# Optimization experiments

Hardware: AMD Instinct MI355X
Metric: run time of the kernel (lower is better)

## Reference

```python
import jax, jax.numpy as jnp
import numpy as np
from jax import lax

C, K, G = 256, 3, 8
CG = C // G          # group channels
P = K * K            # sampling points per group
STRIDE, PAD, DIL = 1, 1, 1
OFFSET_SCALE = 1.0
EPS = 1e-5


def setup_inputs() -> dict:
    key = jax.random.key(0)
    ks = jax.random.split(key, 8)
    N, H, W = 4, 64, 64
    return {
        "x": jax.random.normal(ks[0], (N, C, H, W), jnp.float32),
        "dw_w": jax.random.normal(ks[1], (C, 1, K, K), jnp.float32) * 0.1,
        "dw_b": jax.random.normal(ks[2], (C,), jnp.float32) * 0.01,
        "gn_g": jnp.ones((C,), jnp.float32),
        "gn_b": jnp.zeros((C,), jnp.float32),
        "off_w": jax.random.normal(ks[3], (C, G * P * 2), jnp.float32) * 0.01,
        "off_b": jax.random.normal(ks[4], (G * P * 2,), jnp.float32) * 0.1,
        "mask_w": jax.random.normal(ks[5], (C, G * P), jnp.float32) * 0.02,
        "mask_b": jax.random.normal(ks[6], (G * P,), jnp.float32) * 0.02,
    }


def _dcnv3_core(x_nhwc, offset, mask):
    # x_nhwc (N,H,W,C); offset (N,Ho,Wo,G*P*2); mask (N,Ho,Wo,G*P) already softmaxed
    inp = jnp.pad(x_nhwc, ((0, 0), (PAD, PAD), (PAD, PAD), (0, 0)))
    N, Hp, Wp, _ = inp.shape
    Ho = (Hp - (DIL * (K - 1) + 1)) // STRIDE + 1
    Wo = (Wp - (DIL * (K - 1) + 1)) // STRIDE + 1
    base = (DIL * (K - 1)) // 2 + 0.5
    ref_y = (base + jnp.arange(Ho, dtype=jnp.float32) * STRIDE) / Hp  # (Ho,)
    ref_x = (base + jnp.arange(Wo, dtype=jnp.float32) * STRIDE) / Wp  # (Wo,)
    # dilation grid; flatten order p = iw*K + ih (matches torch meshgrid(x,y) ij)
    kvals = jnp.arange(K, dtype=jnp.float32) * DIL - (DIL * (K - 1)) // 2
    gx = jnp.repeat(kvals, K) / Wp  # (P,)
    gy = jnp.tile(kvals, K) / Hp    # (P,)
    off = offset.reshape(N, Ho, Wo, G, P, 2)
    # normalized sampling locations in [0,1] (then grid_sample convention 2*loc-1)
    loc_x = ref_x[None, None, :, None, None] + gx * OFFSET_SCALE + off[..., 0] * OFFSET_SCALE / Wp
    loc_y = ref_y[None, :, None, None, None] + gy * OFFSET_SCALE + off[..., 1] * OFFSET_SCALE / Hp
    # pixel coords, align_corners=False: px = loc*size - 0.5
    px = loc_x * Wp - 0.5
    py = loc_y * Hp - 0.5
    x0 = jnp.floor(px)
    y0 = jnp.floor(py)
    wx = px - x0
    wy = py - y0
    x0i = x0.astype(jnp.int32)
    y0i = y0.astype(jnp.int32)

    inp_flat = inp.reshape(N, Hp * Wp, G, CG)
    n_idx = jnp.arange(N)[:, None, None, None, None]
    g_idx = jnp.arange(G)[None, None, None, :, None]

    def gather(yi, xi):
        # zeros padding: clamp index, zero out-of-bounds corners
        valid = (yi >= 0) & (yi < Hp) & (xi >= 0) & (xi < Wp)
        idx = jnp.clip(yi, 0, Hp - 1) * Wp + jnp.clip(xi, 0, Wp - 1)
        v = inp_flat[n_idx, idx, g_idx]  # (N,Ho,Wo,G,P,CG)
        return v * valid[..., None]

    m = mask.reshape(N, Ho, Wo, G, P)
    out = jnp.zeros((N, Ho, Wo, G, CG), jnp.float32)
    for dy, dx, w in ((0, 0, (1 - wy) * (1 - wx)), (0, 1, (1 - wy) * wx),
                      (1, 0, wy * (1 - wx)), (1, 1, wy * wx)):
        v = gather(y0i + dy, x0i + dx)
        out = out + jnp.einsum('nhwgp,nhwgpc->nhwgc', m * w, v)
    return out.reshape(N, Ho, Wo, G * CG)


def reference(x, dw_w, dw_b, gn_g, gn_b, off_w, off_b, mask_w, mask_b):
    N, _, H, W = x.shape
    # depthwise 3x3 conv (groups=channels)
    x1 = lax.conv_general_dilated(
        x, dw_w, (1, 1), [((K - 1) // 2, (K - 1) // 2)] * 2,
        dimension_numbers=('NCHW', 'OIHW', 'NCHW'), feature_group_count=C)
    x1 = x1 + dw_b[None, :, None, None]
    # GroupNorm with num_groups=1: normalize over (C,H,W) per sample
    mu = jnp.mean(x1, axis=(1, 2, 3), keepdims=True)
    var = jnp.mean((x1 - mu) ** 2, axis=(1, 2, 3), keepdims=True)
    x1 = (x1 - mu) * lax.rsqrt(var + EPS)
    x1 = x1 * gn_g[None, :, None, None] + gn_b[None, :, None, None]
    x1 = jax.nn.gelu(x1, approximate=False)
    x1 = jnp.transpose(x1, (0, 2, 3, 1))  # NHWC
    offset = x1 @ off_w + off_b                                  # (N,H,W,G*P*2)
    mask = jax.nn.softmax((x1 @ mask_w + mask_b).reshape(N, H, W, G, P), axis=-1)
    mask = mask.reshape(N, H, W, G * P)
    out = _dcnv3_core(jnp.transpose(x, (0, 2, 3, 1)), offset, mask)
    return jnp.transpose(out, (0, 3, 1, 2))  # back to NCHW
```

## Files before the change

kernel.cpp:

```cpp
#include <hip/hip_runtime.h>
#include <math.h>

#define NB   4
#define CH   256
#define HW   4096
#define NCOL 216
#define MTOT 16384
#define CHW  1048576
#define EPSV 1e-5f

#define OFF_NHWC 0
#define NHWCSZ   (NB*HW*CH/2)
#define OFF_OM   (OFF_NHWC + NHWCSZ)
#define OMSZ     (MTOT*NCOL/2)
#define OFF_AB   (OFF_OM + OMSZ)
#define ABSZ     (MTOT*CH/2)
#define OFF_WB   (OFF_AB + ABSZ)
#define WBSZ     (CH*CH/2)
#define OFF_BI   (OFF_WB + WBSZ)
#define OFF_PT   (OFF_BI + 256)

typedef short bf16x8 __attribute__((ext_vector_type(8)));
typedef float f32x4  __attribute__((ext_vector_type(4)));

__device__ __forceinline__ unsigned short f2bf(float f) {
    unsigned int u = __builtin_bit_cast(unsigned int, f);
    u += 0x7fffu + ((u >> 16) & 1u);
    return (unsigned short)(u >> 16);
}

__device__ __forceinline__ float bf2f(unsigned short s) {
    return __builtin_bit_cast(float, (unsigned int)s << 16);
}

__global__ __launch_bounds__(256) void conv_prep_kernel(
    const float* __restrict__ x, const float* __restrict__ dw_w,
    const float* __restrict__ dw_b,
    const float* __restrict__ off_w, const float* __restrict__ off_b,
    const float* __restrict__ mask_w, const float* __restrict__ mask_b,
    unsigned short* __restrict__ A, unsigned short* __restrict__ inp_nhwc,
    unsigned short* __restrict__ Wc_bt, float* __restrict__ bias,
    float* __restrict__ partials) {
    __shared__ float xs[32 * 108];
    __shared__ unsigned short tb[32 * 36];
    __shared__ float rs1[256], rs2[256];
    int b = blockIdx.x;
    int tid = threadIdx.x;
    if (b < 256) {
        int k = b, n = tid;
        float v = 0.f;
        if (n < 144)      v = off_w[k * 144 + n];
        else if (n < 216) v = mask_w[k * 72 + (n - 144)];
        Wc_bt[(size_t)n * 256 + k] = f2bf(v);
        if (b == 0) {
            float bb = 0.f;
            if (n < 144)      bb = off_b[n];
            else if (n < 216) bb = mask_b[n - 144];
            bias[n] = bb;
        }
    }
    int ct  = b & 7;
    int hwt = (b >> 3) & 127;
    int n   = b >> 10;
    int c0 = ct * 32;
    int hw0 = hwt * 32;
    int h  = hw0 >> 6;
    int w0 = hw0 & 63;
    const float* xb = x + ((size_t)n * CH + c0) * HW;
    for (int it = 0; it < 13; ++it) {
        int q = it * 256 + tid;
        if (q < 3264) {
            int cl = q / 102;
            int rr = q - cl * 102;
            int r  = rr / 34;
            int i  = rr - r * 34;
            int gh = h - 1 + r;
            int gw = w0 - 1 + i;
            float v = 0.f;
            if (gh >= 0 && gh < 64 && gw >= 0 && gw < 64)
                v = xb[(size_t)cl * HW + gh * 64 + gw];
            xs[cl * 108 + r * 36 + i] = v;
        }
    }
    __syncthreads();
    int wl = tid & 31;
    int cbase = (tid >> 5) * 4;
    float s1 = 0.f, s2 = 0.f;
    ushort4 o;
    unsigned short ov[4];
#pragma unroll
    for (int j = 0; j < 4; ++j) {
        int c = c0 + cbase + j;
        float acc = dw_b[c];
        const float* wk = dw_w + c * 9;
#pragma unroll
        for (int r = 0; r < 3; ++r)
#pragma unroll
            for (int kx = 0; kx < 3; ++kx)
                acc = fmaf(xs[(cbase + j) * 108 + r * 36 + wl + kx], wk[r * 3 + kx], acc);
        s1 += acc; s2 += acc * acc;
        ov[j] = f2bf(acc);
    }
    o.x = ov[0]; o.y = ov[1]; o.z = ov[2]; o.w = ov[3];
    *(ushort4*)&tb[wl * 36 + cbase] = o;
    rs1[tid] = s1; rs2[tid] = s2;
    {
        int r2 = tid >> 3, cg = tid & 7;
        ushort4 rv;
        rv.x = f2bf(xs[(cg * 4 + 0) * 108 + 36 + r2 + 1]);
        rv.y = f2bf(xs[(cg * 4 + 1) * 108 + 36 + r2 + 1]);
        rv.z = f2bf(xs[(cg * 4 + 2) * 108 + 36 + r2 + 1]);
        rv.w = f2bf(xs[(cg * 4 + 3) * 108 + 36 + r2 + 1]);
        *(ushort4*)&inp_nhwc[((size_t)(n * HW + hw0 + r2)) * 256 + c0 + cg * 4] = rv;
    }
    __syncthreads();
    for (int s = 128; s > 0; s >>= 1) {
        if (tid < s) { rs1[tid] += rs1[tid + s]; rs2[tid] += rs2[tid + s]; }
        __syncthreads();
    }
    if (tid == 0) {
        partials[2 * b]     = rs1[0];
        partials[2 * b + 1] = rs2[0];
    }
    int r2 = tid >> 3, cg = tid & 7;
    ushort4 w4 = *(const ushort4*)&tb[r2 * 36 + cg * 4];
    *(ushort4*)&A[((size_t)(n * HW + hw0 + r2)) * 256 + c0 + cg * 4] = w4;
}

#define LDK 72
__global__ __launch_bounds__(256) void gemm_fused_kernel(
    const unsigned short* __restrict__ A, const unsigned short* __restrict__ Bt,
    const float* __restrict__ bias, const float* __restrict__ partials,
    const float* __restrict__ gn_g, const float* __restrict__ gn_b,
    unsigned short* __restrict__ offmask) {
    __shared__ unsigned short As[32 * LDK];
    __shared__ unsigned short Bs[256 * LDK];
    __shared__ float red1[256], red2[256];
    int m0 = blockIdx.x * 32;
    int n = m0 >> 12;
    int tid = threadIdx.x, lane = tid & 63, wid = tid >> 6;
    float s1 = 0.f, s2 = 0.f;
    for (int i = tid; i < 1024; i += 256) {
        s1 += partials[2 * (n * 1024 + i)];
        s2 += partials[2 * (n * 1024 + i) + 1];
    }
    red1[tid] = s1; red2[tid] = s2;
    __syncthreads();
    for (int st = 128; st > 0; st >>= 1) {
        if (tid < st) { red1[tid] += red1[tid + st]; red2[tid] += red2[tid + st]; }
        __syncthreads();
    }
    float mean = red1[0] * (1.f / (float)CHW);
    float var  = red2[0] * (1.f / (float)CHW) - mean * mean;
    float rsig = rsqrtf(var + EPSV);
    f32x4 acc[2][4] = {};
    for (int k0 = 0; k0 < 256; k0 += 64) {
        {
            int row = tid >> 3, kk0 = (tid & 7) * 8;
            union { uint4 u; unsigned short s[8]; } in, ou;
            in.u = *(const uint4*)&A[((size_t)(m0 + row)) * 256 + k0 + kk0];
#pragma unroll
            for (int j = 0; j < 8; ++j) {
                int ch = k0 + kk0 + j;
                float v = bf2f(in.s[j]);
                v = (v - mean) * rsig * gn_g[ch] + gn_b[ch];
                v = 0.5f * v * (1.0f + erff(v * 0.70710678118654752f));
                ou.s[j] = f2bf(v);
            }
            *(uint4*)&As[row * LDK + kk0] = ou.u;
        }
#pragma unroll
        for (int i = 0; i < 8; ++i) {
            int q = i * 256 + tid;
            int mm = q >> 3, kk = (q & 7) * 8;
            *(uint4*)&Bs[mm * LDK + kk] = *(const uint4*)&Bt[(size_t)mm * 256 + k0 + kk];
        }
        __syncthreads();
#pragma unroll
        for (int kh = 0; kh < 2; ++kh) {
            bf16x8 af[2], bfr[4];
#pragma unroll
            for (int mi = 0; mi < 2; ++mi)
                af[mi] = *(const bf16x8*)&As[(mi * 16 + (lane & 15)) * LDK + kh * 32 + (lane >> 4) * 8];
#pragma unroll
            for (int nj = 0; nj < 4; ++nj)
                bfr[nj] = *(const bf16x8*)&Bs[(wid * 64 + nj * 16 + (lane & 15)) * LDK + kh * 32 + (lane >> 4) * 8];
#pragma unroll
            for (int mi = 0; mi < 2; ++mi)
#pragma unroll
                for (int nj = 0; nj < 4; ++nj)
                    acc[mi][nj] = __builtin_amdgcn_mfma_f32_16x16x32_bf16(
                        af[mi], bfr[nj], acc[mi][nj], 0, 0, 0);
        }
        __syncthreads();
    }
#pragma unroll
    for (int nj = 0; nj < 4; ++nj) {
        int col = wid * 64 + nj * 16 + (lane & 15);
        if (col < NCOL) {
            float bcol = bias[col];
#pragma unroll
            for (int mi = 0; mi < 2; ++mi)
#pragma unroll
                for (int r = 0; r < 4; ++r) {
                    int row = m0 + mi * 16 + (lane >> 4) * 4 + r;
                    offmask[(size_t)row * NCOL + col] = f2bf(acc[mi][nj][r] + bcol);
                }
        }
    }
}

__global__ __launch_bounds__(256) void dcn_out_kernel(
    const unsigned short* __restrict__ inp_nhwc, const unsigned short* __restrict__ offmask,
    float* __restrict__ out) {
    __shared__ float lom[16 * 216];
    __shared__ float ot[16 * 260];
    int tid = threadIdx.x, lane = tid & 63, wid = tid >> 6;
    int pix0 = blockIdx.x * 16;
    int n = pix0 >> 12;
    int hwb = pix0 & 4095;
    {
        const unsigned int* om2 = (const unsigned int*)(offmask + (size_t)pix0 * NCOL);
        for (int i = tid; i < 16 * NCOL / 2; i += 256) {
            unsigned int v = om2[i];
            lom[2 * i]     = bf2f((unsigned short)(v & 0xffffu));
            lom[2 * i + 1] = bf2f((unsigned short)(v >> 16));
        }
    }
    __syncthreads();
    int ph = lane >> 5;
    int l  = lane & 31;
    int g  = l >> 2;
    int ch0 = l * 8;
    const unsigned short* base = inp_nhwc + (size_t)n * HW * 256;
#pragma unroll
    for (int it = 0; it < 2; ++it) {
        int pixloc = it * 8 + wid * 2 + ph;
        int hw = hwb + pixloc;
        int h = hw >> 6, w = hw & 63;
        const float* lm = &lom[pixloc * NCOL];
        float lg[9];
        float mx = -1e30f;
#pragma unroll
        for (int p = 0; p < 9; ++p) { lg[p] = lm[144 + g * 9 + p]; mx = fmaxf(mx, lg[p]); }
        float sum = 0.f;
#pragma unroll
        for (int p = 0; p < 9; ++p) { lg[p] = __expf(lg[p] - mx); sum += lg[p]; }
        float rs = 1.0f / sum;
        float acc[8] = {};
#pragma unroll
        for (int p = 0; p < 9; ++p) {
            float ox = lm[g * 18 + p * 2];
            float oy = lm[g * 18 + p * 2 + 1];
            float px = (float)(w + (p / 3)) + ox;
            float py = (float)(h + (p % 3)) + oy;
            float xf = floorf(px), yf = floorf(py);
            float wx = px - xf, wy = py - yf;
            int x0 = (int)xf, y0 = (int)yf;
            float m = lg[p] * rs;
            float w00 = m * (1.f - wy) * (1.f - wx);
            float w01 = m * (1.f - wy) * wx;
            float w10 = m * wy * (1.f - wx);
            float w11 = m * wy * wx;
#pragma unroll
            for (int corner = 0; corner < 4; ++corner) {
                int yi = y0 + (corner >> 1);
                int xi = x0 + (corner & 1);
                float cw = (corner == 0) ? w00 : (corner == 1) ? w01 : (corner == 2) ? w10 : w11;
                bool valid = (yi >= 1) & (yi <= 64) & (xi >= 1) & (xi <= 64);
                int yc = min(max(yi, 1), 64) - 1;
                int xc = min(max(xi, 1), 64) - 1;
                bf16x8 v = *(const bf16x8*)&base[((size_t)yc * 64 + xc) * 256 + ch0];
                float f = valid ? cw : 0.f;
#pragma unroll
                for (int j = 0; j < 8; ++j)
                    acc[j] = fmaf(f, bf2f((unsigned short)v[j]), acc[j]);
            }
        }
        *(float4*)&ot[pixloc * 260 + ch0]     = make_float4(acc[0], acc[1], acc[2], acc[3]);
        *(float4*)&ot[pixloc * 260 + ch0 + 4] = make_float4(acc[4], acc[5], acc[6], acc[7]);
    }
    __syncthreads();
    int px = tid & 15, crow = tid >> 4;
#pragma unroll
    for (int cc = 0; cc < 16; ++cc) {
        int c = cc * 16 + crow;
        out[((size_t)(n * CH + c)) * HW + hwb + px] = ot[px * 260 + c];
    }
}

extern "C" void kernel_launch(void* const* d_in, const int* in_sizes, int n_in,
                              void* d_out, int out_size, void* d_ws, size_t ws_size,
                              hipStream_t stream) {
    const float* x      = (const float*)d_in[0];
    const float* dw_w   = (const float*)d_in[1];
    const float* dw_b   = (const float*)d_in[2];
    const float* gn_g   = (const float*)d_in[3];
    const float* gn_b   = (const float*)d_in[4];
    const float* off_w  = (const float*)d_in[5];
    const float* off_b  = (const float*)d_in[6];
    const float* mask_w = (const float*)d_in[7];
    const float* mask_b = (const float*)d_in[8];
    float* out = (float*)d_out;

    float* ws = (float*)d_ws;
    unsigned short* inp_nhwc = (unsigned short*)(ws + OFF_NHWC);
    unsigned short* offmask  = (unsigned short*)(ws + OFF_OM);
    unsigned short* Abf   = (unsigned short*)(ws + OFF_AB);
    unsigned short* Wc_bt = (unsigned short*)(ws + OFF_WB);
    float* bias     = ws + OFF_BI;
    float* partials = ws + OFF_PT;

    conv_prep_kernel<<<4096, 256, 0, stream>>>(x, dw_w, dw_b, off_w, off_b,
                                               mask_w, mask_b, Abf, inp_nhwc,
                                               Wc_bt, bias, partials);
    gemm_fused_kernel<<<512, 256, 0, stream>>>(Abf, Wc_bt, bias, partials,
                                               gn_g, gn_b, offmask);
    dcn_out_kernel<<<1024, 256, 0, stream>>>(inp_nhwc, offmask, out);
}
```

Before: 144.5 us.

## Split GN stats into own kernel, retile GEMM, swizzle smaller DCN blocks

Moves the per-sample GroupNorm statistic reduction out of every GEMM block into a tiny separate kernel, so each GEMM block reads only two precomputed floats. The GEMM now uses 512-thread blocks over 64 rows, with each wave covering a 64x32 tile, which halves the number of times the shared B matrix is loaded. The DCN output kernel uses 8 pixels per block over twice as many blocks, with a block-index swizzle that interleaves samples to spread the gather traffic. The costs are an extra kernel launch and smaller output write bursts per block.

Measured after the change: 146.1 us. No clear change (+1.1%).

```diff
diff --git a/kernel.cpp b/kernel.cpp
--- a/kernel.cpp
+++ b/kernel.cpp
@@ -127,33 +127,43 @@
     *(ushort4*)&A[((size_t)(n * HW + hw0 + r2)) * 256 + c0 + cg * 4] = w4;
 }
 
-#define LDK 72
-__global__ __launch_bounds__(256) void gemm_fused_kernel(
-    const unsigned short* __restrict__ A, const unsigned short* __restrict__ Bt,
-    const float* __restrict__ bias, const float* __restrict__ partials,
-    const float* __restrict__ gn_g, const float* __restrict__ gn_b,
-    unsigned short* __restrict__ offmask) {
-    __shared__ unsigned short As[32 * LDK];
-    __shared__ unsigned short Bs[256 * LDK];
-    __shared__ float red1[256], red2[256];
-    int m0 = blockIdx.x * 32;
-    int n = m0 >> 12;
-    int tid = threadIdx.x, lane = tid & 63, wid = tid >> 6;
+__global__ __launch_bounds__(256) void stats_kernel(
+    const float* __restrict__ partials, float* __restrict__ stats) {
+    __shared__ float r1[256], r2[256];
+    int n = blockIdx.x, tid = threadIdx.x;
     float s1 = 0.f, s2 = 0.f;
     for (int i = tid; i < 1024; i += 256) {
         s1 += partials[2 * (n * 1024 + i)];
         s2 += partials[2 * (n * 1024 + i) + 1];
     }
-    red1[tid] = s1; red2[tid] = s2;
-    __syncthreads();
-    for (int st = 128; st > 0; st >>= 1) {
-        if (tid < st) { red1[tid] += red1[tid + st]; red2[tid] += red2[tid + st]; }
+    r1[tid] = s1; r2[tid] = s2;
+    __syncthreads();
+    for (int s = 128; s > 0; s >>= 1) {
+        if (tid < s) { r1[tid] += r1[tid + s]; r2[tid] += r2[tid + s]; }
         __syncthreads();
     }
-    float mean = red1[0] * (1.f / (float)CHW);
-    float var  = red2[0] * (1.f / (float)CHW) - mean * mean;
-    float rsig = rsqrtf(var + EPSV);
-    f32x4 acc[2][4] = {};
+    if (tid == 0) {
+        float mean = r1[0] * (1.f / (float)CHW);
+        float var  = r2[0] * (1.f / (float)CHW) - mean * mean;
+        stats[2 * n]     = mean;
+        stats[2 * n + 1] = rsqrtf(var + EPSV);
+    }
+}
+
+#define LDK 72
+__global__ __launch_bounds__(512) void gemm_fused_kernel(
+    const unsigned short* __restrict__ A, const unsigned short* __restrict__ Bt,
+    const float* __restrict__ bias, const float* __restrict__ stats,
+    const float* __restrict__ gn_g, const float* __restrict__ gn_b,
+    unsigned short* __restrict__ offmask) {
+    __shared__ unsigned short As[64 * LDK];
+    __shared__ unsigned short Bs[256 * LDK];
+    int m0 = blockIdx.x * 64;
+    int n = m0 >> 12;
+    int tid = threadIdx.x, lane = tid & 63, wid = tid >> 6;
+    float mean = stats[2 * n];
+    float rsig = stats[2 * n + 1];
+    f32x4 acc[4][2] = {};
     for (int k0 = 0; k0 < 256; k0 += 64) {
         {
             int row = tid >> 3, kk0 = (tid & 7) * 8;
@@ -170,37 +180,37 @@
             *(uint4*)&As[row * LDK + kk0] = ou.u;
         }
 #pragma unroll
-        for (int i = 0; i < 8; ++i) {
-            int q = i * 256 + tid;
+        for (int i = 0; i < 4; ++i) {
+            int q = i * 512 + tid;
             int mm = q >> 3, kk = (q & 7) * 8;
             *(uint4*)&Bs[mm * LDK + kk] = *(const uint4*)&Bt[(size_t)mm * 256 + k0 + kk];
         }
         __syncthreads();
 #pragma unroll
         for (int kh = 0; kh < 2; ++kh) {
-            bf16x8 af[2], bfr[4];
-#pragma unroll
-            for (int mi = 0; mi < 2; ++mi)
+            bf16x8 af[4], bfr[2];
+#pragma unroll
+            for (int mi = 0; mi < 4; ++mi)
                 af[mi] = *(const bf16x8*)&As[(mi * 16 + (lane & 15)) * LDK + kh * 32 + (lane >> 4) * 8];
 #pragma unroll
-            for (int nj = 0; nj < 4; ++nj)
-                bfr[nj] = *(const bf16x8*)&Bs[(wid * 64 + nj * 16 + (lane & 15)) * LDK + kh * 32 + (lane >> 4) * 8];
-#pragma unroll
-            for (int mi = 0; mi < 2; ++mi)
-#pragma unroll
-                for (int nj = 0; nj < 4; ++nj)
+            for (int nj = 0; nj < 2; ++nj)
+                bfr[nj] = *(const bf16x8*)&Bs[(wid * 32 + nj * 16 + (lane & 15)) * LDK + kh * 32 + (lane >> 4) * 8];
+#pragma unroll
+            for (int mi = 0; mi < 4; ++mi)
+#pragma unroll
+                for (int nj = 0; nj < 2; ++nj)
                     acc[mi][nj] = __builtin_amdgcn_mfma_f32_16x16x32_bf16(
                         af[mi], bfr[nj], acc[mi][nj], 0, 0, 0);
         }
         __syncthreads();
     }
 #pragma unroll
-    for (int nj = 0; nj < 4; ++nj) {
-        int col = wid * 64 + nj * 16 + (lane & 15);
+    for (int nj = 0; nj < 2; ++nj) {
+        int col = wid * 32 + nj * 16 + (lane & 15);
         if (col < NCOL) {
             float bcol = bias[col];
 #pragma unroll
-            for (int mi = 0; mi < 2; ++mi)
+            for (int mi = 0; mi < 4; ++mi)
 #pragma unroll
                 for (int r = 0; r < 4; ++r) {
                     int row = m0 + mi * 16 + (lane >> 4) * 4 + r;
@@ -213,78 +223,76 @@
 __global__ __launch_bounds__(256) void dcn_out_kernel(
     const unsigned short* __restrict__ inp_nhwc, const unsigned short* __restrict__ offmask,
     float* __restrict__ out) {
-    __shared__ float lom[16 * 216];
-    __shared__ float ot[16 * 260];
-    int tid = threadIdx.x, lane = tid & 63, wid = tid >> 6;
-    int pix0 = blockIdx.x * 16;
+    __shared__ float lom[8 * 216];
+    __shared__ float ot[8 * 260];
+    int bid = blockIdx.x;
+    int swz = (bid & 7) * 256 + (bid >> 3);
+    int tid = threadIdx.x;
+    int pix0 = swz * 8;
     int n = pix0 >> 12;
     int hwb = pix0 & 4095;
     {
         const unsigned int* om2 = (const unsigned int*)(offmask + (size_t)pix0 * NCOL);
-        for (int i = tid; i < 16 * NCOL / 2; i += 256) {
+        for (int i = tid; i < 8 * NCOL / 2; i += 256) {
             unsigned int v = om2[i];
             lom[2 * i]     = bf2f((unsigned short)(v & 0xffffu));
             lom[2 * i + 1] = bf2f((unsigned short)(v >> 16));
         }
     }
     __syncthreads();
-    int ph = lane >> 5;
-    int l  = lane & 31;
+    int pixloc = tid >> 5;
+    int l  = tid & 31;
     int g  = l >> 2;
     int ch0 = l * 8;
     const unsigned short* base = inp_nhwc + (size_t)n * HW * 256;
-#pragma unroll
-    for (int it = 0; it < 2; ++it) {
-        int pixloc = it * 8 + wid * 2 + ph;
-        int hw = hwb + pixloc;
-        int h = hw >> 6, w = hw & 63;
-        const float* lm = &lom[pixloc * NCOL];
-        float lg[9];
-        float mx = -1e30f;
-#pragma unroll
-        for (int p = 0; p < 9; ++p) { lg[p] = lm[144 + g * 9 + p]; mx = fmaxf(mx, lg[p]); }
-        float sum = 0.f;
-#pragma unroll
-        for (int p = 0; p < 9; ++p) { lg[p] = __expf(lg[p] - mx); sum += lg[p]; }
-        float rs = 1.0f / sum;
-        float acc[8] = {};
-#pragma unroll
-        for (int p = 0; p < 9; ++p) {
-            float ox = lm[g * 18 + p * 2];
-            float oy = lm[g * 18 + p * 2 + 1];
-            float px = (float)(w + (p / 3)) + ox;
-            float py = (float)(h + (p % 3)) + oy;
-            float xf = floorf(px), yf = floorf(py);
-            float wx = px - xf, wy = py - yf;
-            int x0 = (int)xf, y0 = (int)yf;
-            float m = lg[p] * rs;
-            float w00 = m * (1.f - wy) * (1.f - wx);
-            float w01 = m * (1.f - wy) * wx;
-            float w10 = m * wy * (1.f - wx);
-            float w11 = m * wy * wx;
-#pragma unroll
-            for (int corner = 0; corner < 4; ++corner) {
-                int yi = y0 + (corner >> 1);
-                int xi = x0 + (corner & 1);
-                float cw = (corner == 0) ? w00 : (corner == 1) ? w01 : (corner == 2) ? w10 : w11;
-                bool valid = (yi >= 1) & (yi <= 64) & (xi >= 1) & (xi <= 64);
-                int yc = min(max(yi, 1), 64) - 1;
-                int xc = min(max(xi, 1), 64) - 1;
-                bf16x8 v = *(const bf16x8*)&base[((size_t)yc * 64 + xc) * 256 + ch0];
-                float f = valid ? cw : 0.f;
-#pragma unroll
-                for (int j = 0; j < 8; ++j)
-                    acc[j] = fmaf(f, bf2f((unsigned short)v[j]), acc[j]);
-            }
-        }
-        *(float4*)&ot[pixloc * 260 + ch0]     = make_float4(acc[0], acc[1], acc[2], acc[3]);
-        *(float4*)&ot[pixloc * 260 + ch0 + 4] = make_float4(acc[4], acc[5], acc[6], acc[7]);
-    }
-    __syncthreads();
-    int px = tid & 15, crow = tid >> 4;
-#pragma unroll
-    for (int cc = 0; cc < 16; ++cc) {
-        int c = cc * 16 + crow;
+    int hw = hwb + pixloc;
+    int h = hw >> 6, w = hw & 63;
+    const float* lm = &lom[pixloc * NCOL];
+    float lg[9];
+    float mx = -1e30f;
+#pragma unroll
+    for (int p = 0; p < 9; ++p) { lg[p] = lm[144 + g * 9 + p]; mx = fmaxf(mx, lg[p]); }
+    float sum = 0.f;
+#pragma unroll
+    for (int p = 0; p < 9; ++p) { lg[p] = __expf(lg[p] - mx); sum += lg[p]; }
+    float rs = 1.0f / sum;
+    float acc[8] = {};
+#pragma unroll
+    for (int p = 0; p < 9; ++p) {
+        float ox = lm[g * 18 + p * 2];
+        float oy = lm[g * 18 + p * 2 + 1];
+        float px = (float)(w + (p / 3)) + ox;
+        float py = (float)(h + (p % 3)) + oy;
+        float xf = floorf(px), yf = floorf(py);
+        float wx = px - xf, wy = py - yf;
+        int x0 = (int)xf, y0 = (int)yf;
+        float m = lg[p] * rs;
+        float w00 = m * (1.f - wy) * (1.f - wx);
+        float w01 = m * (1.f - wy) * wx;
+        float w10 = m * wy * (1.f - wx);
+        float w11 = m * wy * wx;
+#pragma unroll
+        for (int corner = 0; corner < 4; ++corner) {
+            int yi = y0 + (corner >> 1);
+            int xi = x0 + (corner & 1);
+            float cw = (corner == 0) ? w00 : (corner == 1) ? w01 : (corner == 2) ? w10 : w11;
+            bool valid = (yi >= 1) & (yi <= 64) & (xi >= 1) & (xi <= 64);
+            int yc = min(max(yi, 1), 64) - 1;
+            int xc = min(max(xi, 1), 64) - 1;
+            bf16x8 v = *(const bf16x8*)&base[((size_t)yc * 64 + xc) * 256 + ch0];
+            float f = valid ? cw : 0.f;
+#pragma unroll
+            for (int j = 0; j < 8; ++j)
+                acc[j] = fmaf(f, bf2f((unsigned short)v[j]), acc[j]);
+        }
+    }
+    *(float4*)&ot[pixloc * 260 + ch0]     = make_float4(acc[0], acc[1], acc[2], acc[3]);
+    *(float4*)&ot[pixloc * 260 + ch0 + 4] = make_float4(acc[4], acc[5], acc[6], acc[7]);
+    __syncthreads();
+    int px = tid & 7, crow = tid >> 3;
+#pragma unroll
+    for (int cc = 0; cc < 8; ++cc) {
+        int c = cc * 32 + crow;
         out[((size_t)(n * CH + c)) * HW + hwb + px] = ot[px * 260 + c];
     }
 }
@@ -310,11 +318,13 @@
     unsigned short* Wc_bt = (unsigned short*)(ws + OFF_WB);
     float* bias     = ws + OFF_BI;
     float* partials = ws + OFF_PT;
+    float* stats    = ws + OFF_BI + 240;
 
     conv_prep_kernel<<<4096, 256, 0, stream>>>(x, dw_w, dw_b, off_w, off_b,
                                                mask_w, mask_b, Abf, inp_nhwc,
                                                Wc_bt, bias, partials);
-    gemm_fused_kernel<<<512, 256, 0, stream>>>(Abf, Wc_bt, bias, partials,
+    stats_kernel<<<4, 256, 0, stream>>>(partials, stats);
+    gemm_fused_kernel<<<256, 512, 0, stream>>>(Abf, Wc_bt, bias, stats,
                                                gn_g, gn_b, offmask);
-    dcn_out_kernel<<<1024, 256, 0, stream>>>(inp_nhwc, offmask, out);
-}
+    dcn_out_kernel<<<2048, 256, 0, stream>>>(inp_nhwc, offmask, out);
+}
```
